# Kernel optimization log

Measured on AMD Instinct MI355X. Metric: run time of the kernel, lower is better.

The kernel has to match this reference:

```python
import jax, jax.numpy as jnp
import numpy as np

HEADS = 16
HEAD_DIM = 64
EMB = 1024
B, S = 4, 2048
SCALE = 1.0 / 8.0  # fixed constant in the original code
MASK_PENALTY = -50.0  # original adds -50 * upper_triangular, not -inf


def setup_inputs() -> dict:
    key = jax.random.key(0)
    ks = jax.random.split(key, 5)
    x = jax.random.normal(ks[0], (B, S, EMB), dtype=jnp.float32)
    Wq = jax.random.normal(ks[1], (EMB, HEADS * HEAD_DIM), dtype=jnp.float32) * 0.02
    Wk = jax.random.normal(ks[2], (EMB, HEADS * HEAD_DIM), dtype=jnp.float32) * 0.02
    Wv = jax.random.normal(ks[3], (EMB, HEADS * HEAD_DIM), dtype=jnp.float32) * 0.02
    Wr = jax.random.normal(ks[4], (HEADS * HEAD_DIM, EMB), dtype=jnp.float32) * 0.02
    return {"x": x, "Wq": Wq, "Wk": Wk, "Wv": Wv, "Wr": Wr}


def reference(x, Wq, Wk, Wv, Wr):
    b, s, _ = x.shape
    # project and split heads: [b, s, h, d]
    q = (x @ Wq).reshape(b, s, HEADS, HEAD_DIM)
    k = (x @ Wk).reshape(b, s, HEADS, HEAD_DIM)
    v = (x @ Wv).reshape(b, s, HEADS, HEAD_DIM)
    # scores: [b, h, s, s]
    scores = SCALE * jnp.einsum('bqhd,bkhd->bhqk', q, k)
    # causal additive mask: -50 on strictly-upper triangle (faithful to original)
    causal = jnp.triu(jnp.ones((s, s), dtype=x.dtype), k=1)
    scores = scores + MASK_PENALTY * causal
    attn = jax.nn.softmax(scores, axis=-1)
    out = jnp.einsum('bhqk,bkhd->bqhd', attn, v).reshape(b, s, HEADS * HEAD_DIM)
    return out @ Wr
```

## Files before the change

kernel.cpp:

```cpp
#include <hip/hip_runtime.h>

typedef _Float16 f16;
typedef _Float16 f16x8 __attribute__((ext_vector_type(8)));
typedef _Float16 f16x4 __attribute__((ext_vector_type(4)));
typedef float f32x4 __attribute__((ext_vector_type(4)));

#define MFMA16(A, B, C) __builtin_amdgcn_mfma_f32_16x16x32_f16((A), (B), (C), 0, 0, 0)

__device__ __forceinline__ void async16(void* lds, const void* gp) {
    __builtin_amdgcn_global_load_lds(
        (__attribute__((address_space(1))) void*)(gp),
        (__attribute__((address_space(3))) void*)(lds), 16, 0, 0);
}

__global__ __launch_bounds__(256) void k_convert(const float* __restrict__ in,
                                                 f16* __restrict__ out, int n) {
    int i = (blockIdx.x * 256 + threadIdx.x) * 4;
    if (i + 3 < n) {
        float4 v = *(const float4*)(in + i);
        f16x4 o = {(f16)v.x, (f16)v.y, (f16)v.z, (f16)v.w};
        *(f16x4*)(out + i) = o;
    }
}

__global__ __launch_bounds__(256) void k_transpose_w4(const float* __restrict__ Wq,
                                                      const float* __restrict__ Wk,
                                                      const float* __restrict__ Wv,
                                                      const float* __restrict__ Wr,
                                                      f16* __restrict__ Wqkvt,
                                                      f16* __restrict__ Wrt) {
    __shared__ float tile[32][33];
    int z = blockIdx.z;
    const float* W = (z == 0) ? Wq : (z == 1) ? Wk : (z == 2) ? Wv : Wr;
    f16* Wt = (z == 3) ? Wrt : Wqkvt + z * 1048576;
    int c0 = blockIdx.x * 32, r0 = blockIdx.y * 32;
    int tx = threadIdx.x, ty = threadIdx.y;
#pragma unroll
    for (int j = 0; j < 32; j += 8)
        tile[ty + j][tx] = W[(r0 + ty + j) * 1024 + c0 + tx];
    __syncthreads();
#pragma unroll
    for (int j = 0; j < 32; j += 8)
        Wt[(c0 + ty + j) * 1024 + r0 + tx] = (f16)tile[tx][ty + j];
}

__global__ __launch_bounds__(256) void k_transpose_v(const f16* __restrict__ QKV,
                                                     f16* __restrict__ Vt) {
    __shared__ f16 tile[32][33];
    int s0 = blockIdx.x * 32;
    int d0 = blockIdx.y * 32;
    int bh = blockIdx.z;
    int b = bh >> 4, h = bh & 15;
    int tx = threadIdx.x, ty = threadIdx.y;
#pragma unroll
    for (int j = 0; j < 32; j += 8)
        tile[ty + j][tx] = QKV[(b * 2048 + s0 + ty + j) * 3072 + 2048 + h * 64 + d0 + tx];
    __syncthreads();
#pragma unroll
    for (int j = 0; j < 32; j += 8)
        Vt[(bh * 64 + d0 + ty + j) * 2048 + s0 + tx] = tile[tx][ty + j];
}

template <bool OUT_F16>
__global__ __launch_bounds__(256) void k_gemm_bt(const f16* __restrict__ A,
                                                 const f16* __restrict__ Bt,
                                                 void* __restrict__ Cv,
                                                 int M, int N, int K) {
    __shared__ f16 As[128][32];
    __shared__ f16 Bs[128][32];
    int t = threadIdx.x;
    int lane = t & 63, w = t >> 6;
    int wm = (w >> 1) * 64, wn = (w & 1) * 64;
    int m0 = blockIdx.y * 128, n0 = blockIdx.x * 128;
    int ln = lane & 15, g = lane >> 4;

    int lin0 = w * 128 + lane, lin1 = lin0 + 64;
    int r0 = lin0 >> 2, c0 = (lin0 & 3) ^ ((r0 >> 1) & 3);
    int r1 = lin1 >> 2, c1 = (lin1 & 3) ^ ((r1 >> 1) & 3);
    const f16* gA0 = A + (size_t)(m0 + r0) * K + c0 * 8;
    const f16* gA1 = A + (size_t)(m0 + r1) * K + c1 * 8;
    const f16* gB0 = Bt + (size_t)(n0 + r0) * K + c0 * 8;
    const f16* gB1 = Bt + (size_t)(n0 + r1) * K + c1 * 8;
    f16* lA0 = &As[0][0] + w * 1024;
    f16* lB0 = &Bs[0][0] + w * 1024;

    f32x4 acc[4][4] = {};
    int sw = (ln >> 1) & 3;

    for (int k0 = 0; k0 < K; k0 += 32) {
        __syncthreads();
        async16(lA0, gA0 + k0);
        async16(lA0 + 512, gA1 + k0);
        async16(lB0, gB0 + k0);
        async16(lB0 + 512, gB1 + k0);
        __syncthreads();
        f16x8 af[4], bf[4];
#pragma unroll
        for (int i = 0; i < 4; i++) {
            af[i] = *(const f16x8*)&As[wm + i * 16 + ln][(g ^ sw) * 8];
            bf[i] = *(const f16x8*)&Bs[wn + i * 16 + ln][(g ^ sw) * 8];
        }
#pragma unroll
        for (int mt = 0; mt < 4; mt++)
#pragma unroll
            for (int nt = 0; nt < 4; nt++)
                acc[mt][nt] = MFMA16(af[mt], bf[nt], acc[mt][nt]);
    }

    int rg = g * 4;
#pragma unroll
    for (int mt = 0; mt < 4; mt++)
#pragma unroll
        for (int nt = 0; nt < 4; nt++)
#pragma unroll
            for (int r = 0; r < 4; r++) {
                int row = m0 + wm + mt * 16 + rg + r;
                int col = n0 + wn + nt * 16 + ln;
                float v = acc[mt][nt][r];
                if (OUT_F16)
                    ((f16*)Cv)[(size_t)row * N + col] = (f16)v;
                else
                    ((float*)Cv)[(size_t)row * N + col] = v;
            }
}

__global__ __launch_bounds__(256, 2) void k_attn(const f16* __restrict__ QKV,
                                                 const f16* __restrict__ Vt,
                                                 f16* __restrict__ Ob) {
    __shared__ f16 Ks[64][72];
    __shared__ f16 Vs[64][72];
    __shared__ f16 Ps[128][72];
    int pi = blockIdx.x, bh = blockIdx.y;
    int b = bh >> 4, h = bh & 15;
    int t = threadIdx.x, lane = t & 63, wq = t >> 6;
    int ln = lane & 15, g = lane >> 4, g8 = g * 8, rg = g * 4;

    int c0 = t, c1 = t + 256;
    int kr0 = c0 >> 3, kc0 = (c0 & 7) * 8;
    int kr1 = c1 >> 3, kc1 = (c1 & 7) * 8;
    const f16* Kbase = QKV + (size_t)b * 2048 * 3072 + 1024 + h * 64;
    const f16* Vbase = Vt + (size_t)bh * 64 * 2048;

    const float C_SCL = 0.18033688f;
    const float C_MSK = -72.134752f;
    f16x8 ones;
#pragma unroll
    for (int j = 0; j < 8; j++) ones[j] = (f16)1.f;

    int4 rk0 = *(const int4*)(Kbase + (size_t)kr0 * 3072 + kc0);
    int4 rk1 = *(const int4*)(Kbase + (size_t)kr1 * 3072 + kc1);
    int4 rv0 = *(const int4*)(Vbase + (size_t)kr0 * 2048 + kc0);
    int4 rv1 = *(const int4*)(Vbase + (size_t)kr1 * 2048 + kc1);

    for (int phase = 0; phase < 2; phase++) {
        int qt = (phase == 0) ? (15 - pi) : pi;
        int q0 = qt * 128;
        int nk = q0 / 64 + 2;

        f16x8 bq[2][2];
#pragma unroll
        for (int nt = 0; nt < 2; nt++)
#pragma unroll
            for (int kd = 0; kd < 2; kd++)
                bq[nt][kd] = *(const f16x8*)(QKV +
                    (size_t)(b * 2048 + q0 + wq * 32 + nt * 16 + ln) * 3072 +
                    h * 64 + kd * 32 + g8);

        f32x4 oacc[2][4] = {};
        f32x4 osum[2] = {};

        for (int kt = 0; kt < nk; kt++) {
            int k0 = kt * 64;
            __syncthreads();
            *(int4*)&Ks[kr0][kc0] = rk0;
            *(int4*)&Ks[kr1][kc1] = rk1;
            *(int4*)&Vs[kr0][kc0] = rv0;
            *(int4*)&Vs[kr1][kc1] = rv1;
            if (kt + 1 < nk) {
                int kn = k0 + 64;
                rk0 = *(const int4*)(Kbase + (size_t)(kn + kr0) * 3072 + kc0);
                rk1 = *(const int4*)(Kbase + (size_t)(kn + kr1) * 3072 + kc1);
                rv0 = *(const int4*)(Vbase + (size_t)kr0 * 2048 + kn + kc0);
                rv1 = *(const int4*)(Vbase + (size_t)kr1 * 2048 + kn + kc1);
            } else if (phase == 0) {
                rk0 = *(const int4*)(Kbase + (size_t)kr0 * 3072 + kc0);
                rk1 = *(const int4*)(Kbase + (size_t)kr1 * 3072 + kc1);
                rv0 = *(const int4*)(Vbase + (size_t)kr0 * 2048 + kc0);
                rv1 = *(const int4*)(Vbase + (size_t)kr1 * 2048 + kc1);
            }
            __syncthreads();

            if (k0 > q0 + wq * 32 + 31) continue;

            f32x4 sacc[4][2] = {};
#pragma unroll
            for (int kd = 0; kd < 2; kd++) {
                f16x8 ak[4];
#pragma unroll
                for (int mt = 0; mt < 4; mt++)
                    ak[mt] = *(const f16x8*)&Ks[mt * 16 + ln][kd * 32 + g8];
#pragma unroll
                for (int mt = 0; mt < 4; mt++)
#pragma unroll
                    for (int nt = 0; nt < 2; nt++)
                        sacc[mt][nt] = MFMA16(ak[mt], bq[nt][kd], sacc[mt][nt]);
            }

            bool needs_mask = (k0 + 63 > q0 + wq * 32);
#pragma unroll
            for (int nt = 0; nt < 2; nt++) {
                int q = q0 + wq * 32 + nt * 16 + ln;
#pragma unroll
                for (int mt = 0; mt < 4; mt++) {
                    f16x4 pk;
#pragma unroll
                    for (int r = 0; r < 4; r++) {
                        float e;
                        if (needs_mask) {
                            int kk = k0 + mt * 16 + rg + r;
                            e = __builtin_amdgcn_exp2f(
                                fmaf(sacc[mt][nt][r], C_SCL, (kk > q) ? C_MSK : 0.f));
                        } else {
                            e = __builtin_amdgcn_exp2f(sacc[mt][nt][r] * C_SCL);
                        }
                        pk[r] = (f16)e;
                    }
                    *(f16x4*)&Ps[wq * 32 + nt * 16 + ln][mt * 16 + rg] = pk;
                }
            }

#pragma unroll
            for (int kk = 0; kk < 2; kk++) {
                f16x8 ap[2], bv[4];
#pragma unroll
                for (int mt = 0; mt < 2; mt++)
                    ap[mt] = *(const f16x8*)&Ps[wq * 32 + mt * 16 + ln][kk * 32 + g8];
#pragma unroll
                for (int dt = 0; dt < 4; dt++)
                    bv[dt] = *(const f16x8*)&Vs[dt * 16 + ln][kk * 32 + g8];
#pragma unroll
                for (int mt = 0; mt < 2; mt++) {
#pragma unroll
                    for (int dt = 0; dt < 4; dt++)
                        oacc[mt][dt] = MFMA16(ap[mt], bv[dt], oacc[mt][dt]);
                    osum[mt] = MFMA16(ap[mt], ones, osum[mt]);
                }
            }
        }

#pragma unroll
        for (int mt = 0; mt < 2; mt++)
#pragma unroll
            for (int r = 0; r < 4; r++) {
                float inv = __builtin_amdgcn_rcpf(osum[mt][r]);
                int row = b * 2048 + q0 + wq * 32 + mt * 16 + rg + r;
#pragma unroll
                for (int dt = 0; dt < 4; dt++)
                    Ob[(size_t)row * 1024 + h * 64 + dt * 16 + ln] =
                        (f16)(oacc[mt][dt][r] * inv);
            }
    }
}

extern "C" void kernel_launch(void* const* d_in, const int* in_sizes, int n_in,
                              void* d_out, int out_size, void* d_ws, size_t ws_size,
                              hipStream_t stream) {
    const float* x = (const float*)d_in[0];
    const float* Wq = (const float*)d_in[1];
    const float* Wk = (const float*)d_in[2];
    const float* Wv = (const float*)d_in[3];
    const float* Wr = (const float*)d_in[4];
    float* out = (float*)d_out;

    f16* ws = (f16*)d_ws;
    f16* xb    = ws;
    f16* Wqkvt = xb + 8388608;
    f16* Wrt   = Wqkvt + 3145728;
    f16* QKVb  = Wrt + 1048576;
    f16* Vtb   = QKVb + 25165824;
    f16* Obuf  = Vtb + 8388608;

    k_convert<<<8192, 256, 0, stream>>>(x, xb, 8388608);
    dim3 tb(32, 8);
    k_transpose_w4<<<dim3(32, 32, 4), tb, 0, stream>>>(Wq, Wk, Wv, Wr, Wqkvt, Wrt);
    k_gemm_bt<true><<<dim3(24, 64), 256, 0, stream>>>(xb, Wqkvt, QKVb, 8192, 3072, 1024);
    k_transpose_v<<<dim3(64, 2, 64), tb, 0, stream>>>(QKVb, Vtb);
    k_attn<<<dim3(8, 64), 256, 0, stream>>>(QKVb, Vtb, Obuf);
    k_gemm_bt<false><<<dim3(8, 64), 256, 0, stream>>>(Obuf, Wrt, out, 8192, 1024, 1024);
}
```

Before: 283.2 us.

## Split causal attention KV range across two blocks and merge partial outputs

Each query tile's key range is now split between two blocks, and the grid doubles to 16x64. Each block writes a normalized partial output plus its row sum, and a new merge kernel combines the two halves weighted by those sums. The launch bound is raised to 4 blocks per CU. This aims to raise parallelism and balance work across the causal triangle, at the cost of an extra kernel, extra global traffic for the partials, and possible register pressure.

```diff
diff --git a/kernel.cpp b/kernel.cpp
--- a/kernel.cpp
+++ b/kernel.cpp
@@ -124,9 +124,10 @@
             }
 }
 
-__global__ __launch_bounds__(256, 2) void k_attn(const f16* __restrict__ QKV,
+__global__ __launch_bounds__(256, 4) void k_attn(const f16* __restrict__ QKV,
                                                  const f16* __restrict__ Vt,
-                                                 f16* __restrict__ Ob) {
+                                                 f16* __restrict__ Opart,
+                                                 float* __restrict__ Rsum) {
     __shared__ f16 Ks[64][72];
     __shared__ f16 Vs[64][72];
     __shared__ f16 Ps[128][72];
@@ -153,9 +154,10 @@
     int4 rv1 = *(const int4*)(Vbase + (size_t)kr1 * 2048 + kc1);
 
     for (int phase = 0; phase < 2; phase++) {
-        int qt = (phase == 0) ? (15 - pi) : pi;
+        int qt  = phase ? pi : 15 - pi;
+        int ktB = phase ? pi + 1 : 0;
+        int ktE = phase ? 2 * pi + 2 : 16 - pi;
         int q0 = qt * 128;
-        int nk = q0 / 64 + 2;
 
         f16x8 bq[2][2];
 #pragma unroll
@@ -169,24 +171,25 @@
         f32x4 oacc[2][4] = {};
         f32x4 osum[2] = {};
 
-        for (int kt = 0; kt < nk; kt++) {
+        for (int kt = ktB; kt < ktE; kt++) {
             int k0 = kt * 64;
             __syncthreads();
             *(int4*)&Ks[kr0][kc0] = rk0;
             *(int4*)&Ks[kr1][kc1] = rk1;
             *(int4*)&Vs[kr0][kc0] = rv0;
             *(int4*)&Vs[kr1][kc1] = rv1;
-            if (kt + 1 < nk) {
+            if (kt + 1 < ktE) {
                 int kn = k0 + 64;
                 rk0 = *(const int4*)(Kbase + (size_t)(kn + kr0) * 3072 + kc0);
                 rk1 = *(const int4*)(Kbase + (size_t)(kn + kr1) * 3072 + kc1);
                 rv0 = *(const int4*)(Vbase + (size_t)kr0 * 2048 + kn + kc0);
                 rv1 = *(const int4*)(Vbase + (size_t)kr1 * 2048 + kn + kc1);
             } else if (phase == 0) {
-                rk0 = *(const int4*)(Kbase + (size_t)kr0 * 3072 + kc0);
-                rk1 = *(const int4*)(Kbase + (size_t)kr1 * 3072 + kc1);
-                rv0 = *(const int4*)(Vbase + (size_t)kr0 * 2048 + kc0);
-                rv1 = *(const int4*)(Vbase + (size_t)kr1 * 2048 + kc1);
+                int kn = (pi + 1) * 64;
+                rk0 = *(const int4*)(Kbase + (size_t)(kn + kr0) * 3072 + kc0);
+                rk1 = *(const int4*)(Kbase + (size_t)(kn + kr1) * 3072 + kc1);
+                rv0 = *(const int4*)(Vbase + (size_t)kr0 * 2048 + kn + kc0);
+                rv1 = *(const int4*)(Vbase + (size_t)kr1 * 2048 + kn + kc1);
             }
             __syncthreads();
 
@@ -248,18 +251,42 @@
             }
         }
 
+        int u = (bh * 16 + qt) * 2 + phase;
 #pragma unroll
         for (int mt = 0; mt < 2; mt++)
 #pragma unroll
             for (int r = 0; r < 4; r++) {
-                float inv = __builtin_amdgcn_rcpf(osum[mt][r]);
-                int row = b * 2048 + q0 + wq * 32 + mt * 16 + rg + r;
+                float rs = osum[mt][r];
+                float inv = __builtin_amdgcn_rcpf(fmaxf(rs, 1e-30f));
+                int q = wq * 32 + mt * 16 + rg + r;
+                if (ln == 0) Rsum[u * 128 + q] = rs;
 #pragma unroll
                 for (int dt = 0; dt < 4; dt++)
-                    Ob[(size_t)row * 1024 + h * 64 + dt * 16 + ln] =
+                    Opart[(size_t)u * 8192 + q * 64 + dt * 16 + ln] =
                         (f16)(oacc[mt][dt][r] * inv);
             }
     }
+}
+
+__global__ __launch_bounds__(256) void k_merge(const f16* __restrict__ Op,
+                                               const float* __restrict__ Rs,
+                                               f16* __restrict__ Ob) {
+    int idx = blockIdx.x * 256 + threadIdx.x;
+    int d8 = idx & 7;
+    int q  = (idx >> 3) & 127;
+    int qt = (idx >> 10) & 15;
+    int bh = idx >> 14;
+    int b = bh >> 4, hd = bh & 15;
+    int u0 = (bh * 16 + qt) * 2;
+    float rs0 = Rs[u0 * 128 + q], rs1 = Rs[(u0 + 1) * 128 + q];
+    float inv = __builtin_amdgcn_rcpf(rs0 + rs1);
+    f16x8 o0 = *(const f16x8*)(Op + (size_t)u0 * 8192 + q * 64 + d8 * 8);
+    f16x8 o1 = *(const f16x8*)(Op + (size_t)(u0 + 1) * 8192 + q * 64 + d8 * 8);
+    f16x8 o;
+#pragma unroll
+    for (int j = 0; j < 8; j++)
+        o[j] = (f16)((rs0 * (float)o0[j] + rs1 * (float)o1[j]) * inv);
+    *(f16x8*)(Ob + (size_t)(b * 2048 + qt * 128 + q) * 1024 + hd * 64 + d8 * 8) = o;
 }
 
 extern "C" void kernel_launch(void* const* d_in, const int* in_sizes, int n_in,
@@ -279,12 +306,15 @@
     f16* QKVb  = Wrt + 1048576;
     f16* Vtb   = QKVb + 25165824;
     f16* Obuf  = Vtb + 8388608;
+    f16* Opart = Obuf + 8388608;
+    float* Rsum = (float*)(Opart + 16777216);
 
     k_convert<<<8192, 256, 0, stream>>>(x, xb, 8388608);
     dim3 tb(32, 8);
     k_transpose_w4<<<dim3(32, 32, 4), tb, 0, stream>>>(Wq, Wk, Wv, Wr, Wqkvt, Wrt);
     k_gemm_bt<true><<<dim3(24, 64), 256, 0, stream>>>(xb, Wqkvt, QKVb, 8192, 3072, 1024);
     k_transpose_v<<<dim3(64, 2, 64), tb, 0, stream>>>(QKVb, Vtb);
-    k_attn<<<dim3(8, 64), 256, 0, stream>>>(QKVb, Vtb, Obuf);
+    k_attn<<<dim3(16, 64), 256, 0, stream>>>(QKVb, Vtb, Opart, Rsum);
+    k_merge<<<4096, 256, 0, stream>>>(Opart, Rsum, Obuf);
     k_gemm_bt<false><<<dim3(8, 64), 256, 0, stream>>>(Obuf, Wrt, out, 8192, 1024, 1024);
 }
```

New measurement: 302.3 us. +6.7%, slower.
